# Optimization experiments

Hardware: AMD Instinct MI355X
Metric: run time of the kernel (lower is better)

Reference implementation:

```python
import jax, jax.numpy as jnp
import numpy as np

EPS_SINK = 0.01   # SinkhornDistance eps
N_ITERS = 20      # fixed iteration count (original: max 100 with host-side early exit)
BN_EPS = 1e-5


def _conv(x, w, b):
    # NCHW 3x3 (or 1x1) conv, SAME padding
    y = jax.lax.conv_general_dilated(x, w, (1, 1), 'SAME',
                                     dimension_numbers=('NCHW', 'OIHW', 'NCHW'))
    return y + b[None, :, None, None]


def _bn_train(x, gamma, beta):
    # BatchNorm2d in training mode: batch statistics over (N,H,W)
    m = jnp.mean(x, axis=(0, 2, 3), keepdims=True)
    v = jnp.var(x, axis=(0, 2, 3), keepdims=True)
    return gamma[None, :, None, None] * (x - m) * jax.lax.rsqrt(v + BN_EPS) + beta[None, :, None, None]


def _calc_mean_std(f, eps=1e-5):
    m = jnp.mean(f, axis=(2, 3), keepdims=True)
    s = jnp.sqrt(jnp.var(f, axis=(2, 3), keepdims=True) + eps)
    return m, s


def _sinkhorn_pi(x, y, eps):
    # x: [b, n, d] content points, y: [b, m, d] style points. Cosine-distance cost.
    xn = x / jnp.linalg.norm(x, axis=-1, keepdims=True)
    yn = y / jnp.linalg.norm(y, axis=-1, keepdims=True)
    C = 1.0 - jnp.einsum('bnd,bmd->bnm', xn, yn)          # [b, n, m]
    b, n, m = C.shape
    log_mu = jnp.log(jnp.full((b, n), 1.0 / n) + 1e-8)
    log_nu = jnp.log(jnp.full((b, m), 1.0 / m) + 1e-8)

    def Mmat(u, v):
        # (-C + u_i + v_j) / eps
        return (-C + u[..., None] + v[..., None, :]) / eps

    def step(carry, _):
        u, v = carry
        u = eps * (log_mu - jax.scipy.special.logsumexp(Mmat(u, v), axis=-1)) + u
        v = eps * (log_nu - jax.scipy.special.logsumexp(Mmat(u, v), axis=-2)) + v
        return (u, v), None

    (u, v), _ = jax.lax.scan(step, (jnp.zeros((b, n)), jnp.zeros((b, m))), None, length=N_ITERS)
    return jnp.exp(Mmat(u, v))                             # transport plan pi


def setup_inputs() -> dict:
    key = jax.random.key(0)
    ks = jax.random.split(key, 16)
    bs, dim, h, w = 4, 512, 32, 32
    s = 0.05
    return {
        'content_feat': jax.random.normal(ks[0], (bs, dim, h, w), jnp.float32),
        'style_feat':   jax.random.normal(ks[1], (bs, dim, h, w), jnp.float32),
        # alpha_predictor (version 1): conv(1024->256,3x3) ReLU BN, conv(256->256,3x3) ReLU BN, conv(256->512,3x3)
        'w1': jax.random.normal(ks[2], (256, 1024, 3, 3), jnp.float32) * s,
        'b1': jnp.zeros((256,), jnp.float32),
        'g1': jnp.ones((256,), jnp.float32),
        'be1': jnp.zeros((256,), jnp.float32),
        'w2': jax.random.normal(ks[3], (256, 256, 3, 3), jnp.float32) * s,
        'b2': jnp.zeros((256,), jnp.float32),
        'g2': jnp.ones((256,), jnp.float32),
        'be2': jnp.zeros((256,), jnp.float32),
        'w3': jax.random.normal(ks[4], (512, 256, 3, 3), jnp.float32) * s,
        'b3': jnp.zeros((512,), jnp.float32),
        # stand-in decoder head: 3x3 conv 512->3 (decoder is an external injected module)
        'dec_w': jax.random.normal(ks[5], (3, 512, 3, 3), jnp.float32) * s,
        'dec_b': jnp.zeros((3,), jnp.float32),
    }


def reference(content_feat, style_feat, w1, b1, g1, be1, w2, b2, g2, be2, w3, b3, dec_w, dec_b):
    bs, dim, h, w = content_feat.shape
    cf = content_feat.reshape(bs, dim, h * w).transpose(0, 2, 1)   # [b, hw, d]
    sf = style_feat.reshape(bs, dim, h * w).transpose(0, 2, 1)
    pi = _sinkhorn_pi(cf, sf, EPS_SINK) * (h * w)                  # style_assign: pi * h * w
    t = jnp.einsum('bnm,bmd->bnd', pi, sf).transpose(0, 2, 1).reshape(bs, dim, h, w)
    cm, cs = _calc_mean_std(content_feat)
    c_normed = (content_feat - cm) / cs
    a = _bn_train(jax.nn.relu(_conv(jnp.concatenate([t, content_feat], axis=1), w1, b1)), g1, be1)
    a = _bn_train(jax.nn.relu(_conv(a, w2, b2)), g2, be2)
    alpha = _conv(a, w3, b3)
    t = alpha * c_normed + t
    g_t = _conv(t, dec_w, dec_b)
    return g_t
```

## Files before the change

kernel.cpp:

```cpp
#include <hip/hip_runtime.h>

typedef unsigned short u16;
typedef unsigned int u32;
typedef unsigned long long u64;
typedef float f32x4 __attribute__((ext_vector_type(4)));
typedef short bf16x8 __attribute__((ext_vector_type(8)));

#define DEV static __device__ __forceinline__

DEV float bf2f(u16 u){ union{float f; u32 i;} x; x.i = ((u32)u) << 16; return x.f; }
DEV u16 f2bf(float f){ union{float f; u32 i;} x; x.f = f; u32 u = x.i;
  return (u16)((u + 0x7fffu + ((u >> 16) & 1u)) >> 16); }
DEV u16 f2h(float f){ _Float16 h = (_Float16)f; u16 u; __builtin_memcpy(&u, &h, 2); return u; }
DEV float h2f(u16 u){ _Float16 h; __builtin_memcpy(&h, &u, 2); return (float)h; }
DEV uint4 pack8(const u16* s){ uint4 v;
  v.x = (u32)s[0] | ((u32)s[1]<<16); v.y = (u32)s[2] | ((u32)s[3]<<16);
  v.z = (u32)s[4] | ((u32)s[5]<<16); v.w = (u32)s[6] | ((u32)s[7]<<16); return v; }
DEV f32x4 mfma16(bf16x8 a, bf16x8 b, f32x4 c){
  return __builtin_amdgcn_mfma_f32_16x16x32_bf16(a, b, c, 0, 0, 0);
}
DEV bf16x8 ldfrag(const u16* p){ return *(const bf16x8*)p; }

DEV void st_agent(float* p, float v){
  __hip_atomic_store(p, v, __ATOMIC_RELAXED, __HIP_MEMORY_SCOPE_AGENT); }
DEV float ld_agent(const float* p){
  return __hip_atomic_load(p, __ATOMIC_RELAXED, __HIP_MEMORY_SCOPE_AGENT); }
DEV float2 ld_agent2(const float* p){
  u64 u = __hip_atomic_load((const u64*)p, __ATOMIC_RELAXED, __HIP_MEMORY_SCOPE_AGENT);
  union{u64 u; float2 f;} c; c.u = u; return c.f; }
DEV void st_agent_u32(u32* p, u32 v){
  __hip_atomic_store(p, v, __ATOMIC_RELAXED, __HIP_MEMORY_SCOPE_AGENT); }
DEV u32 ld_agent_u32(const u32* p){
  return __hip_atomic_load(p, __ATOMIC_RELAXED, __HIP_MEMORY_SCOPE_AGENT); }

constexpr float SCL = 144.269504088896341f;
constexpr float LOG2MU = -9.99998522680257f;

constexpr size_t MB = 1ull << 20;
constexpr size_t OFF_G    = 0;
constexpr size_t OFF_GT   = 8*MB;
constexpr size_t OFF_U    = 16*MB;
constexpr size_t OFF_V    = OFF_U   + (16<<10);
constexpr size_t OFF_BAR  = OFF_V   + (16<<10);
constexpr size_t OFF_INS  = OFF_BAR + (16<<10);
constexpr size_t OFF_CNM  = OFF_INS + (16<<10);
constexpr size_t OFF_CNIS = OFF_CNM + (8<<10);
constexpr size_t OFF_BNS  = OFF_CNIS+ (8<<10);
constexpr size_t OFF_PNP  = OFF_BNS + (4<<10);
constexpr size_t OFF_CFH  = 17*MB;
constexpr size_t OFF_CFL  = 21*MB;
constexpr size_t OFF_SFH  = 25*MB;
constexpr size_t OFF_SFL  = 29*MB;
constexpr size_t OFF_SNB  = 33*MB;
constexpr size_t OFF_TN   = 37*MB;
constexpr size_t OFF_TCP  = 45*MB;
constexpr size_t OFF_W1P  = 53*MB;
constexpr size_t OFF_W2P  = OFF_W1P + 9*256*1024*2;
constexpr size_t OFF_W3P  = OFF_W2P + 9*256*256*2;
constexpr size_t OFF_WDP  = OFF_W3P + 9*512*256*2;
constexpr size_t OFF_PIP  = 62*MB;
constexpr size_t OFF_Z1  = 17*MB;
constexpr size_t OFF_A1P = 25*MB;
constexpr size_t OFF_Z2  = 27*MB;
constexpr size_t OFF_A2P = 35*MB;
constexpr size_t OFF_T2P = 17*MB;

__global__ void stats_k(const float* __restrict__ cf, const float* __restrict__ sf,
                        float* __restrict__ cnm, float* __restrict__ cnis,
                        float* __restrict__ part, float* __restrict__ zUV,
                        float* __restrict__ zBNS, u32* __restrict__ zbar,
                        const float* __restrict__ w1, const float* __restrict__ w2,
                        const float* __restrict__ w3, const float* __restrict__ wd,
                        u16* __restrict__ w1p, u16* __restrict__ w2p,
                        u16* __restrict__ w3p, u16* __restrict__ wdp){
  int blk = blockIdx.x;
  if (blk < 2048){
    int bd = blk;
    float4 v = ((const float4*)(cf + (size_t)bd*1024))[threadIdx.x];
    float s = v.x+v.y+v.z+v.w;
    float q = v.x*v.x+v.y*v.y+v.z*v.z+v.w*v.w;
    #pragma unroll
    for (int m = 32; m >= 1; m >>= 1){ s += __shfl_xor(s, m, 64); q += __shfl_xor(q, m, 64); }
    __shared__ float ls[4], lq[4];
    int w = threadIdx.x >> 6;
    if ((threadIdx.x & 63) == 0){ ls[w] = s; lq[w] = q; }
    __syncthreads();
    if (threadIdx.x == 0){
      float S = ls[0]+ls[1]+ls[2]+ls[3], Q = lq[0]+lq[1]+lq[2]+lq[3];
      float mean = S * (1.f/1024.f);
      float var  = Q * (1.f/1024.f) - mean*mean;
      cnm[bd] = mean; cnis[bd] = rsqrtf(var + 1e-5f);
    }
    return;
  }
  if (blk < 2304){
    int rel = blk - 2048;
    int x = rel & 15, y = (rel >> 4) & 7, src = rel >> 7;
    const float* in = src ? sf : cf;
    int p = x*256 + threadIdx.x;
    int b = p >> 10, pp = p & 1023;
    const float* base = in + ((size_t)(b*512 + y*64))*1024 + pp;
    float s = 0.f;
    #pragma unroll 8
    for (int d = 0; d < 64; ++d){ float xx = base[(size_t)d*1024]; s += xx*xx; }
    part[((size_t)(src*8 + y))*4096 + p] = s;
    return;
  }
  if (blk < 2336){
    zUV[(blk - 2304)*256 + threadIdx.x] = 0.f;
    return;
  }
  if (blk < 2340){
    zBNS[(blk - 2336)*256 + threadIdx.x] = 0.f;
    return;
  }
  if (blk < 2356){
    zbar[(blk - 2340)*256 + threadIdx.x] = 0u;
    return;
  }
  int pblk = blk - 2356;
  const float* w; u16* wp; int CI, NCK, rel;
  if (pblk < 512){ w = w1; wp = w1p; CI = 1024; NCK = 32; rel = pblk; }
  else if (pblk < 640){ w = w2; wp = w2p; CI = 256; NCK = 8; rel = pblk - 512; }
  else if (pblk < 896){ w = w3; wp = w3p; CI = 256; NCK = 8; rel = pblk - 640; }
  else {
    int o = (pblk - 896)*256 + threadIdx.x;
    int ci = o & 511; int r = o >> 9; int co = r & 15; int tap = r >> 4;
    wdp[o] = f2bf((co < 3) ? wd[(size_t)(co*512 + ci)*9 + tap] : 0.f);
    return;
  }
  int g = rel / NCK, ck = rel % NCK;
  __shared__ float L[16*288];
  const float* base = w + ((size_t)(g*16)*CI + ck*32)*9;
  #pragma unroll
  for (int i = 0; i < 18; ++i){
    int idx = i*256 + threadIdx.x;
    int row = idx / 288, col = idx - row*288;
    L[row*288 + col] = base[(size_t)row*CI*9 + col];
  }
  __syncthreads();
  u16* dst = wp + ((size_t)(g*NCK + ck)*9)*512;
  #pragma unroll
  for (int i = 0; i < 18; ++i){
    int j = i*256 + threadIdx.x;
    int tap = j >> 9, r = j & 511, lane = r >> 3, e = r & 7;
    int co = lane & 15, cil = ((lane >> 4) & 3)*8 + e;
    dst[j] = f2bf(L[co*288 + cil*9 + tap]);
  }
}

__global__ void tsplit_k(const float* __restrict__ cf, const float* __restrict__ sf,
                         const float* __restrict__ pnp,
                         u16* __restrict__ cfh, u16* __restrict__ cfl,
                         u16* __restrict__ sfh, u16* __restrict__ sfl,
                         u16* __restrict__ tcp, u16* __restrict__ snb){
  __shared__ float tile[64][65];
  int z = blockIdx.z, is_style = z >> 2, b = z & 3;
  const float* src = is_style ? sf : cf;
  u16* hi = is_style ? sfh : cfh;
  u16* lo = is_style ? sfl : cfl;
  int p0 = blockIdx.x*64, d0 = blockIdx.y*64;
  int r = threadIdx.x >> 2, c0 = (threadIdx.x & 3) * 16;
  const float* sp = src + ((size_t)(b*512 + d0 + r))*1024 + p0 + c0;
  float v[16];
  #pragma unroll
  for (int e = 0; e < 4; ++e){
    float4 t4 = ((const float4*)sp)[e];
    v[e*4+0]=t4.x; v[e*4+1]=t4.y; v[e*4+2]=t4.z; v[e*4+3]=t4.w;
  }
  #pragma unroll
  for (int j = 0; j < 16; ++j) tile[r][c0+j] = v[j];
  if (is_style){
    u16 t16[16];
    #pragma unroll
    for (int j = 0; j < 16; ++j) t16[j] = f2bf(v[j]);
    uint4* ap = (uint4*)(snb + ((size_t)(b*512 + d0 + r))*1024 + p0 + c0);
    ap[0] = pack8(t16); ap[1] = pack8(t16+8);
  }
  __syncthreads();
  int pr = r, dc0 = c0;
  float inv;
  {
    const float* pp = pnp + (size_t)(is_style ? 8*4096 : 0) + ((b<<10) + p0 + pr);
    float s = 0.f;
    #pragma unroll
    for (int j = 0; j < 8; ++j) s += pp[j*4096];
    inv = rsqrtf(s);
  }
  u16 h16[16], l16[16], t16[16];
  #pragma unroll
  for (int j = 0; j < 16; ++j){
    float x = tile[dc0+j][pr];
    t16[j] = f2bf(x);
    float xn = x * inv;
    u16 h = f2bf(xn);
    h16[j] = h;
    l16[j] = f2bf(xn - bf2f(h));
  }
  size_t orow = (size_t)((b<<10) + p0 + pr);
  uint4* hp = (uint4*)(hi + orow*512 + d0 + dc0);
  uint4* lp = (uint4*)(lo + orow*512 + d0 + dc0);
  hp[0] = pack8(h16); hp[1] = pack8(h16+8);
  lp[0] = pack8(l16); lp[1] = pack8(l16+8);
  if (!is_style){
    int D = d0 + dc0;
    size_t off = ((size_t)(16 + (D>>5))*4096 + orow)*32 + (D&31);
    *(uint4*)(tcp + off)     = pack8(t16);
    *(uint4*)(tcp + off + 8) = pack8(t16+8);
  }
}

__global__ __launch_bounds__(256) void cgemm_k(const u16* __restrict__ cfh, const u16* __restrict__ cfl,
        const u16* __restrict__ sfh, const u16* __restrict__ sfl,
        u16* __restrict__ G, u16* __restrict__ Gt){
  __shared__ __align__(16) u16 SH[4*128*40];
  u16* Ah = SH;          u16* Al = SH + 5120;
  u16* Bh = SH + 10240;  u16* Bl = SH + 15360;
  int b = blockIdx.z;
  size_t abase = ((size_t)((b<<10) + blockIdx.x*128))*512;
  size_t bbase = ((size_t)((b<<10) + blockIdx.y*128))*512;
  int lane = threadIdx.x & 63, wid = threadIdx.x >> 6;
  int wm = (wid >> 1)*64, wn = (wid & 1)*64;
  int fr = lane & 15, qd = lane >> 4;
  int sr = threadIdx.x >> 1, sc = (threadIdx.x & 1)*16;
  f32x4 acc[4][4] = {};
  for (int kk = 0; kk < 512; kk += 32){
    size_t g0 = (size_t)sr*512 + kk + sc;
    *(uint4*)&Ah[sr*40+sc]   = *(const uint4*)(cfh + abase + g0);
    *(uint4*)&Ah[sr*40+sc+8] = *(const uint4*)(cfh + abase + g0 + 8);
    *(uint4*)&Al[sr*40+sc]   = *(const uint4*)(cfl + abase + g0);
    *(uint4*)&Al[sr*40+sc+8] = *(const uint4*)(cfl + abase + g0 + 8);
    *(uint4*)&Bh[sr*40+sc]   = *(const uint4*)(sfh + bbase + g0);
    *(uint4*)&Bh[sr*40+sc+8] = *(const uint4*)(sfh + bbase + g0 + 8);
    *(uint4*)&Bl[sr*40+sc]   = *(const uint4*)(sfl + bbase + g0);
    *(uint4*)&Bl[sr*40+sc+8] = *(const uint4*)(sfl + bbase + g0 + 8);
    __syncthreads();
    bf16x8 bhf[4], blf[4];
    #pragma unroll
    for (int ni = 0; ni < 4; ++ni){
      bhf[ni] = ldfrag(&Bh[(wn + ni*16 + fr)*40 + qd*8]);
      blf[ni] = ldfrag(&Bl[(wn + ni*16 + fr)*40 + qd*8]);
    }
    #pragma unroll
    for (int mi = 0; mi < 4; ++mi){
      bf16x8 ah = ldfrag(&Ah[(wm + mi*16 + fr)*40 + qd*8]);
      bf16x8 al = ldfrag(&Al[(wm + mi*16 + fr)*40 + qd*8]);
      #pragma unroll
      for (int ni = 0; ni < 4; ++ni){
        acc[mi][ni] = mfma16(ah, bhf[ni], acc[mi][ni]);
        acc[mi][ni] = mfma16(ah, blf[ni], acc[mi][ni]);
        acc[mi][ni] = mfma16(al, bhf[ni], acc[mi][ni]);
      }
    }
    __syncthreads();
  }
  #pragma unroll
  for (int mi = 0; mi < 4; ++mi)
    #pragma unroll
    for (int ni = 0; ni < 4; ++ni)
      #pragma unroll
      for (int rg = 0; rg < 4; ++rg){
        int r = wm + mi*16 + qd*4 + rg;
        int c = wn + ni*16 + fr;
        SH[r*136 + c] = f2h((acc[mi][ni][rg] - 1.f) * SCL);
      }
  __syncthreads();
  size_t gb = (((size_t)b) << 20) + (size_t)(blockIdx.x*128)*1024 + blockIdx.y*128;
  #pragma unroll
  for (int i = 0; i < 8; ++i){
    int idx = i*256 + threadIdx.x;
    int r = idx >> 4, c4 = idx & 15;
    *(uint4*)(G + gb + (size_t)r*1024 + c4*8) = *(const uint4*)&SH[r*136 + c4*8];
  }
  __syncthreads();
  #pragma unroll
  for (int mi = 0; mi < 4; ++mi)
    #pragma unroll
    for (int ni = 0; ni < 4; ++ni)
      #pragma unroll
      for (int rg = 0; rg < 4; ++rg){
        int r = wm + mi*16 + qd*4 + rg;
        int c = wn + ni*16 + fr;
        SH[c*136 + r] = f2h((acc[mi][ni][rg] - 1.f) * SCL);
      }
  __syncthreads();
  size_t gtb = (((size_t)b) << 20) + (size_t)(blockIdx.y*128)*1024 + blockIdx.x*128;
  #pragma unroll
  for (int i = 0; i < 8; ++i){
    int idx = i*256 + threadIdx.x;
    int r = idx >> 4, c4 = idx & 15;
    *(uint4*)(Gt + gtb + (size_t)r*1024 + c4*8) = *(const uint4*)&SH[r*136 + c4*8];
  }
}

__global__ __launch_bounds__(512) void sink_k(const u16* __restrict__ G, const u16* __restrict__ Gt,
        float* __restrict__ U, float* __restrict__ V,
        u32* __restrict__ flags, u16* __restrict__ pip){
  __shared__ __align__(16) u16 LL[2][16*1024];
  int blk = blockIdx.x;
  int b = blk >> 6;
  int sub = blk & 63;
  int rb = sub << 4;
  int tid = threadIdx.x;
  size_t gbase = ((size_t)((b << 10) + rb)) << 10;
  {
    const uint4* g0 = (const uint4*)(G + gbase);
    const uint4* g1 = (const uint4*)(Gt + gbase);
    uint4* d0 = (uint4*)LL[0];
    uint4* d1 = (uint4*)LL[1];
    #pragma unroll
    for (int i = 0; i < 4; ++i){
      d0[i*512 + tid] = g0[i*512 + tid];
      d1[i*512 + tid] = g1[i*512 + tid];
    }
  }
  __syncthreads();
  int wid = tid >> 6, lane = tid & 63;
  float* Ub = U + (b << 10);
  float* Vb = V + (b << 10);
  u32* fgrp = flags + (b << 6)*16;
  u32* fmine = fgrp + sub*16;
  int r0 = wid << 1;
  int cbase = lane << 2;
  int budget = 1 << 21;

  float o0 = 0.f, o1 = 0.f;
  auto dopass = [&](int which, const float* __restrict__ inv, float* __restrict__ outv, int tgt){
    float va[16];
    #pragma unroll
    for (int k = 0; k < 4; ++k){
      #pragma unroll
      for (int j = 0; j < 2; ++j){
        float2 t = ld_agent2(inv + k*256 + cbase + j*2);
        va[k*4 + j*2]     = t.x;
        va[k*4 + j*2 + 1] = t.y;
      }
    }
    #pragma unroll
    for (int rr = 0; rr < 2; ++rr){
      int row = r0 + rr;
      float x[16]; float mx = -3.0e38f;
      #pragma unroll
      for (int k = 0; k < 4; ++k){
        uint2 g2 = *(const uint2*)(&LL[which][row*1024 + k*256 + cbase]);
        float t0 = h2f((u16)(g2.x & 0xffffu)) + va[k*4+0];
        float t1 = h2f((u16)(g2.x >> 16))     + va[k*4+1];
        float t2 = h2f((u16)(g2.y & 0xffffu)) + va[k*4+2];
        float t3 = h2f((u16)(g2.y >> 16))     + va[k*4+3];
        x[k*4+0]=t0; x[k*4+1]=t1; x[k*4+2]=t2; x[k*4+3]=t3;
        mx = fmaxf(mx, fmaxf(fmaxf(t0,t1), fmaxf(t2,t3)));
      }
      #pragma unroll
      for (int m = 32; m >= 1; m >>= 1) mx = fmaxf(mx, __shfl_xor(mx, m, 64));
      float s = 0.f;
      #pragma unroll
      for (int i = 0; i < 16; ++i) s += exp2f(x[i] - mx);
      #pragma unroll
      for (int m = 32; m >= 1; m >>= 1) s += __shfl_xor(s, m, 64);
      float o = LOG2MU - (mx + log2f(s));
      if (rr == 0) o0 = o; else o1 = o;
      if (lane == 0) st_agent(outv + rb + row, o);
    }
    __syncthreads();
    if (tid == 0) st_agent_u32(fmine, (u32)tgt);
    if (tid < 64){
      u32* fl = fgrp + tid*16;
      for (;;){
        u32 v = ld_agent_u32(fl);
        if (__all((int)(v >= (u32)tgt))) break;
        if (--budget < 0) break;
        __builtin_amdgcn_s_sleep(1);
      }
    }
    __syncthreads();
  };

  float ku0 = 0.f, ku1 = 0.f;
  for (int it = 0; it < 20; ++it){
    dopass(0, Vb, Ub, 2*it + 1);
    ku0 = o0; ku1 = o1;
    dopass(1, Ub, Vb, 2*it + 2);
  }

  float va[16];
  #pragma unroll
  for (int k = 0; k < 4; ++k){
    #pragma unroll
    for (int j = 0; j < 2; ++j){
      float2 t = ld_agent2(Vb + k*256 + cbase + j*2);
      va[k*4 + j*2]     = t.x;
      va[k*4 + j*2 + 1] = t.y;
    }
  }
  #pragma unroll
  for (int rr = 0; rr < 2; ++rr){
    int row = r0 + rr;
    float ur = (rr == 0 ? ku0 : ku1) + 10.f;
    size_t orow = ((size_t)((b << 10) + rb + row)) << 10;
    #pragma unroll
    for (int k = 0; k < 4; ++k){
      uint2 g2 = *(const uint2*)(&LL[0][row*1024 + k*256 + cbase]);
      u16 o[4];
      o[0] = f2bf(exp2f(h2f((u16)(g2.x & 0xffffu)) + va[k*4+0] + ur));
      o[1] = f2bf(exp2f(h2f((u16)(g2.x >> 16))     + va[k*4+1] + ur));
      o[2] = f2bf(exp2f(h2f((u16)(g2.y & 0xffffu)) + va[k*4+2] + ur));
      o[3] = f2bf(exp2f(h2f((u16)(g2.y >> 16))     + va[k*4+3] + ur));
      uint2 pk; pk.x = (u32)o[0] | ((u32)o[1]<<16); pk.y = (u32)o[2] | ((u32)o[3]<<16);
      *(uint2*)(pip + orow + k*256 + cbase) = pk;
    }
  }
}

__global__ __launch_bounds__(256) void tgemm_k(const u16* __restrict__ pip,
        const u16* __restrict__ snb, float* __restrict__ tn, u16* __restrict__ tcp){
  __shared__ __align__(16) u16 As[64*40], Bs[128*40];
  int b = blockIdx.z, p0 = blockIdx.x*64, d0 = blockIdx.y*128;
  int tid = threadIdx.x, lane = tid & 63, wid = tid >> 6;
  int wm = (wid >> 1)*32, wn = (wid & 1)*64;
  int fr = lane & 15, qd = lane >> 4;
  int a_r = tid >> 2, a_c = (tid & 3)*8;
  int b_r = tid >> 1, b_c = (tid & 1)*16;
  const u16* Arow = pip + (((size_t)((b<<10) + p0 + a_r)) << 10) + a_c;
  const u16* Brow = snb + (((size_t)(b*512 + d0 + b_r)) << 10) + b_c;
  uint4 pa, pb0, pb1;
  auto issue = [&](int kk){
    pa = *(const uint4*)(Arow + kk);
    const uint4* bp = (const uint4*)(Brow + kk);
    pb0 = bp[0]; pb1 = bp[1];
  };
  f32x4 acc[2][4] = {};
  issue(0);
  for (int kk = 0; kk < 1024; kk += 32){
    *(uint4*)&As[a_r*40 + a_c] = pa;
    *(uint4*)&Bs[b_r*40 + b_c] = pb0;
    *(uint4*)&Bs[b_r*40 + b_c + 8] = pb1;
    __syncthreads();
    if (kk + 32 < 1024) issue(kk + 32);
    bf16x8 bfr[4];
    #pragma unroll
    for (int ni = 0; ni < 4; ++ni) bfr[ni] = ldfrag(&Bs[(wn + ni*16 + fr)*40 + qd*8]);
    #pragma unroll
    for (int mi = 0; mi < 2; ++mi){
      bf16x8 afr = ldfrag(&As[(wm + mi*16 + fr)*40 + qd*8]);
      #pragma unroll
      for (int ni = 0; ni < 4; ++ni) acc[mi][ni] = mfma16(afr, bfr[ni], acc[mi][ni]);
    }
    __syncthreads();
  }
  #pragma unroll
  for (int mi = 0; mi < 2; ++mi)
    #pragma unroll
    for (int ni = 0; ni < 4; ++ni)
      #pragma unroll
      for (int rg = 0; rg < 4; ++rg){
        int p = p0 + wm + mi*16 + qd*4 + rg;
        int d = d0 + wn + ni*16 + fr;
        float vout = acc[mi][ni][rg];
        size_t ro = (size_t)((b<<10) + p);
        tn[ro*512 + d] = vout;
        tcp[((size_t)(d>>5)*4096 + ro)*32 + (d&31)] = f2bf(vout);
      }
}

template<int CI, int CO, int KSPLIT, int MODE>
__global__ __launch_bounds__(256) void conv_k(const u16* __restrict__ inp, const u16* __restrict__ wpk,
        const float* __restrict__ bias, float* __restrict__ fout, u16* __restrict__ bout,
        const u16* __restrict__ tcp, const float* __restrict__ cnm, const float* __restrict__ cnis,
        const float* __restrict__ tn){
  constexpr int NCK_TOT = CI/32, NCK = NCK_TOT/KSPLIT;
  __shared__ __align__(16) u16 As[128*40];
  int b = blockIdx.z & 3, ks = blockIdx.z >> 2;
  int c0 = blockIdx.y*64;
  int r0 = blockIdx.x*2;
  int tid = threadIdx.x, lane = tid & 63, wid = tid >> 6;
  int wm = (wid >> 1)*32, wn = (wid & 1)*32;
  int fr = lane & 15, qd = lane >> 4;
  int ck0 = ks*NCK;
  int hrow = tid >> 1;
  int ah = (tid & 1)*16;
  int gy = r0 - 1 + (hrow >> 5);
  bool a_ok = ((unsigned)gy < 32u);
  size_t arow = (size_t)(b<<10) + (r0-1)*32 + hrow;
  uint4 pa0 = {0,0,0,0}, pa1 = {0,0,0,0};
  auto issueA = [&](int ck){
    if (a_ok){
      const uint4* s = (const uint4*)(inp + ((size_t)(ck0+ck)*4096 + arow)*32 + ah);
      pa0 = s[0]; pa1 = s[1];
    }
  };
  int g0 = (c0 + wn) >> 4;
  const u16* wb0 = wpk + ((size_t)(g0    )*NCK_TOT + ck0)*9*512 + lane*8;
  const u16* wb1 = wpk + ((size_t)(g0 + 1)*NCK_TOT + ck0)*9*512 + lane*8;

  f32x4 acc[2][2] = {};
  issueA(0);
  for (int ck = 0; ck < NCK; ++ck){
    *(uint4*)&As[hrow*40 + ah]     = pa0;
    *(uint4*)&As[hrow*40 + ah + 8] = pa1;
    __syncthreads();
    if (ck + 1 < NCK) issueA(ck + 1);
    #pragma unroll
    for (int tap = 0; tap < 9; ++tap){
      const int dy = tap/3 - 1, dx = tap%3 - 1;
      bf16x8 bf0 = ldfrag(wb0 + (size_t)(ck*9 + tap)*512);
      bf16x8 bf1 = ldfrag(wb1 + (size_t)(ck*9 + tap)*512);
      #pragma unroll
      for (int mi = 0; mi < 2; ++mi){
        int p0w = wm + mi*16;
        int pcol = (p0w & 31) + fr + dx;
        int lr = (p0w >> 5) + dy + 1;
        bool okc = (unsigned)pcol < 32u;
        bf16x8 af = ldfrag(&As[(lr*32 + (okc ? pcol : 0))*40 + qd*8]);
        if (!okc) af = bf16x8(0);
        acc[mi][0] = mfma16(af, bf0, acc[mi][0]);
        acc[mi][1] = mfma16(af, bf1, acc[mi][1]);
      }
    }
    __syncthreads();
  }
  #pragma unroll
  for (int mi = 0; mi < 2; ++mi)
    #pragma unroll
    for (int ni = 0; ni < 2; ++ni)
      #pragma unroll
      for (int rg = 0; rg < 4; ++rg){
        int pp = blockIdx.x*64 + wm + mi*16 + qd*4 + rg;
        int cc = c0 + wn + ni*16 + fr;
        float v = acc[mi][ni][rg];
        size_t ro = (size_t)((b<<10) + pp);
        if (MODE == 0){
          fout[(size_t)ks*4096*CO + ro*CO + cc] = v;
        } else {
          float alpha = v + bias[cc];
          float cn = (bf2f(tcp[((size_t)(16 + (cc>>5))*4096 + ro)*32 + (cc&31)])
                      - cnm[(b<<9) + cc]) * cnis[(b<<9) + cc];
          bout[((size_t)(cc>>5)*4096 + ro)*32 + (cc&31)] = f2bf(alpha*cn + tn[ro*512 + cc]);
        }
      }
}

__global__ __launch_bounds__(512) void dec_k(const u16* __restrict__ t2p, const u16* __restrict__ wdp,
                                             const float* __restrict__ db, float* __restrict__ out){
  __shared__ float wlds[3*4608];
  int tid = threadIdx.x;
  for (int k = tid; k < 3*4608; k += 512){
    int c = k / 4608, rem = k - c*4608;
    int tap = rem >> 9, ci = rem & 511;
    wlds[k] = bf2f(wdp[(size_t)(tap*16 + c)*512 + ci]);
  }
  __syncthreads();
  int b = blockIdx.x >> 5;
  int p = ((blockIdx.x & 31) << 5) + (tid >> 4);
  int sub = tid & 15;
  int py = p >> 5, px = p & 31;
  float a0 = 0.f, a1 = 0.f, a2 = 0.f;
  for (int tap = 0; tap < 9; ++tap){
    int sy = py + tap/3 - 1, sx = px + tap%3 - 1;
    if (((unsigned)sy < 32u) && ((unsigned)sx < 32u)){
      size_t row = (size_t)((b<<10) + (sy<<5) + sx);
      const float* w0 = wlds + tap*512;
      #pragma unroll
      for (int j = 0; j < 4; ++j){
        int ci0 = j*128 + sub*8;
        uint4 v = *(const uint4*)(t2p + ((size_t)(ci0>>5)*4096 + row)*32 + (ci0&31));
        u32 ww[4] = {v.x, v.y, v.z, v.w};
        #pragma unroll
        for (int e = 0; e < 8; ++e){
          float x = bf2f((u16)((e & 1) ? (ww[e>>1] >> 16) : (ww[e>>1] & 0xffffu)));
          a0 += x * w0[ci0 + e];
          a1 += x * w0[4608 + ci0 + e];
          a2 += x * w0[9216 + ci0 + e];
        }
      }
    }
  }
  #pragma unroll
  for (int m = 8; m >= 1; m >>= 1){
    a0 += __shfl_xor(a0, m, 64);
    a1 += __shfl_xor(a1, m, 64);
    a2 += __shfl_xor(a2, m, 64);
  }
  if (sub == 0){
    out[((size_t)(b*3 + 0) << 10) + p] = a0 + db[0];
    out[((size_t)(b*3 + 1) << 10) + p] = a1 + db[1];
    out[((size_t)(b*3 + 2) << 10) + p] = a2 + db[2];
  }
}

__global__ void bn_stats_k(const float* __restrict__ z, const float* __restrict__ bias,
                           float* __restrict__ sums){
  int c = blockIdx.x*64 + (threadIdx.x & 63);
  int w = threadIdx.x >> 6;
  int rbase = blockIdx.y*128 + w*32;
  float bi = bias[c];
  float s = 0.f, q = 0.f;
  for (int i = 0; i < 32; ++i){
    size_t ro = (size_t)(rbase + i)*256 + c;
    float x = fmaxf(z[ro] + z[4096*256 + ro] + bi, 0.f);
    s += x; q += x*x;
  }
  __shared__ float ls[4][64], lq[4][64];
  ls[w][threadIdx.x & 63] = s; lq[w][threadIdx.x & 63] = q;
  __syncthreads();
  if (threadIdx.x < 64){
    float S = ls[0][threadIdx.x]+ls[1][threadIdx.x]+ls[2][threadIdx.x]+ls[3][threadIdx.x];
    float Q = lq[0][threadIdx.x]+lq[1][threadIdx.x]+lq[2][threadIdx.x]+lq[3][threadIdx.x];
    atomicAdd(&sums[blockIdx.x*64 + threadIdx.x], S);
    atomicAdd(&sums[256 + blockIdx.x*64 + threadIdx.x], Q);
  }
}

__global__ void bn_apply_k(const float* __restrict__ z, const float* __restrict__ bias,
                           const float* __restrict__ sums, const float* __restrict__ gamma,
                           const float* __restrict__ beta, u16* __restrict__ ap){
  int idx = blockIdx.x*256 + threadIdx.x;
  float4 va = ((const float4*)z)[idx];
  float4 vb = ((const float4*)(z + 4096*256))[idx];
  int row = idx >> 6;
  int cc0 = (idx << 2) & 255;
  float e[4] = {va.x+vb.x, va.y+vb.y, va.z+vb.z, va.w+vb.w};
  u16 o[4];
  #pragma unroll
  for (int k = 0; k < 4; ++k){
    int c = cc0 + k;
    float mean = sums[c] * (1.f/4096.f);
    float var  = sums[256 + c] * (1.f/4096.f) - mean*mean;
    float sc = gamma[c] * rsqrtf(var + 1e-5f);
    float sh = beta[c] - mean*sc;
    float x = fmaxf(e[k] + bias[c], 0.f);
    o[k] = f2bf(x*sc + sh);
  }
  uint2 pk; pk.x = (u32)o[0] | ((u32)o[1]<<16); pk.y = (u32)o[2] | ((u32)o[3]<<16);
  *(uint2*)(ap + ((size_t)(cc0>>5)*4096 + row)*32 + (cc0&31)) = pk;
}

extern "C" void kernel_launch(void* const* d_in, const int* in_sizes, int n_in,
                              void* d_out, int out_size, void* d_ws, size_t ws_size,
                              hipStream_t stream){
  const float* cf  = (const float*)d_in[0];
  const float* sf  = (const float*)d_in[1];
  const float* w1  = (const float*)d_in[2];
  const float* b1  = (const float*)d_in[3];
  const float* g1  = (const float*)d_in[4];
  const float* be1 = (const float*)d_in[5];
  const float* w2  = (const float*)d_in[6];
  const float* b2  = (const float*)d_in[7];
  const float* g2  = (const float*)d_in[8];
  const float* be2 = (const float*)d_in[9];
  const float* w3  = (const float*)d_in[10];
  const float* b3  = (const float*)d_in[11];
  const float* dw  = (const float*)d_in[12];
  const float* db  = (const float*)d_in[13];

  char* ws = (char*)d_ws;
  u16* G    = (u16*)(ws + OFF_G);
  u16* Gt   = (u16*)(ws + OFF_GT);
  float* U    = (float*)(ws + OFF_U);
  float* V    = (float*)(ws + OFF_V);
  u32* bar    = (u32*)(ws + OFF_BAR);
  float* cnm  = (float*)(ws + OFF_CNM);
  float* cnis = (float*)(ws + OFF_CNIS);
  float* bns1 = (float*)(ws + OFF_BNS);
  float* bns2 = bns1 + 512;
  float* pnp  = (float*)(ws + OFF_PNP);
  u16* cfh = (u16*)(ws + OFF_CFH);
  u16* cfl = (u16*)(ws + OFF_CFL);
  u16* sfh = (u16*)(ws + OFF_SFH);
  u16* sfl = (u16*)(ws + OFF_SFL);
  u16* snb = (u16*)(ws + OFF_SNB);
  float* tn  = (float*)(ws + OFF_TN);
  u16* tcp = (u16*)(ws + OFF_TCP);
  u16* w1p = (u16*)(ws + OFF_W1P);
  u16* w2p = (u16*)(ws + OFF_W2P);
  u16* w3p = (u16*)(ws + OFF_W3P);
  u16* wdp = (u16*)(ws + OFF_WDP);
  u16* pip = (u16*)(ws + OFF_PIP);
  float* z1  = (float*)(ws + OFF_Z1);
  u16*   a1p = (u16*)(ws + OFF_A1P);
  float* z2  = (float*)(ws + OFF_Z2);
  u16*   a2p = (u16*)(ws + OFF_A2P);
  u16*   t2p = (u16*)(ws + OFF_T2P);

  stats_k<<<3540, 256, 0, stream>>>(cf, sf, cnm, cnis, pnp, U, bns1, bar,
                                    w1, w2, w3, dw, w1p, w2p, w3p, wdp);
  tsplit_k<<<dim3(16, 8, 8), 256, 0, stream>>>(cf, sf, pnp, cfh, cfl, sfh, sfl, tcp, snb);

  cgemm_k<<<dim3(8, 8, 4), 256, 0, stream>>>(cfh, cfl, sfh, sfl, G, Gt);

  sink_k<<<256, 512, 0, stream>>>(G, Gt, U, V, bar, pip);

  tgemm_k<<<dim3(16, 4, 4), 256, 0, stream>>>(pip, snb, tn, tcp);

  conv_k<1024, 256, 2, 0><<<dim3(16, 4, 8), 256, 0, stream>>>(
      tcp, w1p, nullptr, z1, nullptr, nullptr, nullptr, nullptr, nullptr);
  bn_stats_k<<<dim3(4, 32), 256, 0, stream>>>(z1, b1, bns1);
  bn_apply_k<<<1024, 256, 0, stream>>>(z1, b1, bns1, g1, be1, a1p);

  conv_k<256, 256, 2, 0><<<dim3(16, 4, 8), 256, 0, stream>>>(
      a1p, w2p, nullptr, z2, nullptr, nullptr, nullptr, nullptr, nullptr);
  bn_stats_k<<<dim3(4, 32), 256, 0, stream>>>(z2, b2, bns2);
  bn_apply_k<<<1024, 256, 0, stream>>>(z2, b2, bns2, g2, be2, a2p);

  conv_k<256, 512, 1, 1><<<dim3(16, 8, 4), 256, 0, stream>>>(
      a2p, w3p, b3, nullptr, t2p, tcp, cnm, cnis, tn);

  dec_k<<<128, 512, 0, stream>>>(t2p, wdp, db, (float*)d_out);

  (void)in_sizes; (void)n_in; (void)out_size; (void)ws_size;
}
```

Before: 393.6 us.

## Overlap content half of conv1 with Sinkhorn blocks; prefetch cgemm tiles

Extra blocks are added to the Sinkhorn kernel launch. They compute the content-channel half of the first 3x3 conv, which depends only on content features, and write it into a second z1 split-K slice while the Sinkhorn blocks iterate. The standalone conv1 launch shrinks its split-K grid to cover only the remaining slice. Separately, the cgemm main loop now register-prefetches the next K tile before computing the current one. The risk is that the Sinkhorn blocks, which use a grid-wide barrier, could be delayed or deadlock if the extra blocks prevent all 256 Sinkhorn blocks from being co-resident.

Result: no change. 389.9 us (-0.9%).

```diff
diff --git a/kernel.cpp b/kernel.cpp
--- a/kernel.cpp
+++ b/kernel.cpp
@@ -23,8 +23,6 @@
 
 DEV void st_agent(float* p, float v){
   __hip_atomic_store(p, v, __ATOMIC_RELAXED, __HIP_MEMORY_SCOPE_AGENT); }
-DEV float ld_agent(const float* p){
-  return __hip_atomic_load(p, __ATOMIC_RELAXED, __HIP_MEMORY_SCOPE_AGENT); }
 DEV float2 ld_agent2(const float* p){
   u64 u = __hip_atomic_load((const u64*)p, __ATOMIC_RELAXED, __HIP_MEMORY_SCOPE_AGENT);
   union{u64 u; float2 f;} c; c.u = u; return c.f; }
@@ -223,18 +221,24 @@
   int wm = (wid >> 1)*64, wn = (wid & 1)*64;
   int fr = lane & 15, qd = lane >> 4;
   int sr = threadIdx.x >> 1, sc = (threadIdx.x & 1)*16;
+  const u16 *pA = cfh + abase, *pB = cfl + abase, *pC = sfh + bbase, *pD = sfl + bbase;
+  uint4 rA0, rA1, rB0, rB1, rC0, rC1, rD0, rD1;
+  auto issue = [&](int kk){
+    size_t g0 = (size_t)sr*512 + kk + sc;
+    rA0 = *(const uint4*)(pA + g0); rA1 = *(const uint4*)(pA + g0 + 8);
+    rB0 = *(const uint4*)(pB + g0); rB1 = *(const uint4*)(pB + g0 + 8);
+    rC0 = *(const uint4*)(pC + g0); rC1 = *(const uint4*)(pC + g0 + 8);
+    rD0 = *(const uint4*)(pD + g0); rD1 = *(const uint4*)(pD + g0 + 8);
+  };
   f32x4 acc[4][4] = {};
+  issue(0);
   for (int kk = 0; kk < 512; kk += 32){
-    size_t g0 = (size_t)sr*512 + kk + sc;
-    *(uint4*)&Ah[sr*40+sc]   = *(const uint4*)(cfh + abase + g0);
-    *(uint4*)&Ah[sr*40+sc+8] = *(const uint4*)(cfh + abase + g0 + 8);
-    *(uint4*)&Al[sr*40+sc]   = *(const uint4*)(cfl + abase + g0);
-    *(uint4*)&Al[sr*40+sc+8] = *(const uint4*)(cfl + abase + g0 + 8);
-    *(uint4*)&Bh[sr*40+sc]   = *(const uint4*)(sfh + bbase + g0);
-    *(uint4*)&Bh[sr*40+sc+8] = *(const uint4*)(sfh + bbase + g0 + 8);
-    *(uint4*)&Bl[sr*40+sc]   = *(const uint4*)(sfl + bbase + g0);
-    *(uint4*)&Bl[sr*40+sc+8] = *(const uint4*)(sfl + bbase + g0 + 8);
-    __syncthreads();
+    *(uint4*)&Ah[sr*40+sc]   = rA0; *(uint4*)&Ah[sr*40+sc+8] = rA1;
+    *(uint4*)&Al[sr*40+sc]   = rB0; *(uint4*)&Al[sr*40+sc+8] = rB1;
+    *(uint4*)&Bh[sr*40+sc]   = rC0; *(uint4*)&Bh[sr*40+sc+8] = rC1;
+    *(uint4*)&Bl[sr*40+sc]   = rD0; *(uint4*)&Bl[sr*40+sc+8] = rD1;
+    __syncthreads();
+    if (kk + 32 < 512) issue(kk + 32);
     bf16x8 bhf[4], blf[4];
     #pragma unroll
     for (int ni = 0; ni < 4; ++ni){
@@ -295,13 +299,68 @@
 
 __global__ __launch_bounds__(512) void sink_k(const u16* __restrict__ G, const u16* __restrict__ Gt,
         float* __restrict__ U, float* __restrict__ V,
-        u32* __restrict__ flags, u16* __restrict__ pip){
+        u32* __restrict__ flags, u16* __restrict__ pip,
+        const u16* __restrict__ cin, const u16* __restrict__ wpk,
+        float* __restrict__ z1out){
   __shared__ __align__(16) u16 LL[2][16*1024];
   int blk = blockIdx.x;
+  int tid = threadIdx.x;
+  if (blk >= 256){
+    u16* As = LL[0];
+    int cbid = blk - 256;
+    int cx = cbid & 15, cy = (cbid >> 4) & 3, b = cbid >> 6;
+    const int NCK_TOT = 32, NCK = 16, ck0 = 16;
+    int c0 = cy*64, r0 = cx*2;
+    int lane = tid & 63, wid = tid >> 6;
+    int wm = (wid >> 2)*32, wn = (wid & 3)*16;
+    int fr = lane & 15, qd = lane >> 4;
+    int hrow = tid >> 2, ah = (tid & 3)*8;
+    int gy = r0 - 1 + (hrow >> 5);
+    bool a_ok = ((unsigned)gy < 32u);
+    size_t arow = (size_t)(b<<10) + (r0-1)*32 + hrow;
+    uint4 pa = {0,0,0,0};
+    auto issueA = [&](int ck){
+      if (a_ok) pa = *(const uint4*)(cin + ((size_t)(ck0+ck)*4096 + arow)*32 + ah);
+    };
+    int g0 = (c0 + wn) >> 4;
+    const u16* wb = wpk + ((size_t)g0*NCK_TOT + ck0)*9*512 + lane*8;
+    f32x4 acc[2] = {};
+    issueA(0);
+    for (int ck = 0; ck < NCK; ++ck){
+      *(uint4*)&As[hrow*40 + ah] = pa;
+      __syncthreads();
+      if (ck + 1 < NCK) issueA(ck + 1);
+      #pragma unroll
+      for (int tap = 0; tap < 9; ++tap){
+        const int dy = tap/3 - 1, dx = tap%3 - 1;
+        bf16x8 bf = ldfrag(wb + (size_t)(ck*9 + tap)*512);
+        #pragma unroll
+        for (int mi = 0; mi < 2; ++mi){
+          int p0w = wm + mi*16;
+          int pcol = (p0w & 31) + fr + dx;
+          int lr = (p0w >> 5) + dy + 1;
+          bool okc = (unsigned)pcol < 32u;
+          bf16x8 af = ldfrag(&As[(lr*32 + (okc ? pcol : 0))*40 + qd*8]);
+          if (!okc) af = bf16x8(0);
+          acc[mi] = mfma16(af, bf, acc[mi]);
+        }
+      }
+      __syncthreads();
+    }
+    #pragma unroll
+    for (int mi = 0; mi < 2; ++mi)
+      #pragma unroll
+      for (int rg = 0; rg < 4; ++rg){
+        int pp = cx*64 + wm + mi*16 + qd*4 + rg;
+        int cc = c0 + wn + fr;
+        size_t ro = (size_t)((b<<10) + pp);
+        z1out[(size_t)4096*256 + ro*256 + cc] = acc[mi][rg];
+      }
+    return;
+  }
   int b = blk >> 6;
   int sub = blk & 63;
   int rb = sub << 4;
-  int tid = threadIdx.x;
   size_t gbase = ((size_t)((b << 10) + rb)) << 10;
   {
     const uint4* g0 = (const uint4*)(G + gbase);
@@ -687,11 +746,11 @@
 
   cgemm_k<<<dim3(8, 8, 4), 256, 0, stream>>>(cfh, cfl, sfh, sfl, G, Gt);
 
-  sink_k<<<256, 512, 0, stream>>>(G, Gt, U, V, bar, pip);
+  sink_k<<<512, 512, 0, stream>>>(G, Gt, U, V, bar, pip, tcp, w1p, z1);
 
   tgemm_k<<<dim3(16, 4, 4), 256, 0, stream>>>(pip, snb, tn, tcp);
 
-  conv_k<1024, 256, 2, 0><<<dim3(16, 4, 8), 256, 0, stream>>>(
+  conv_k<1024, 256, 2, 0><<<dim3(16, 4, 4), 256, 0, stream>>>(
       tcp, w1p, nullptr, z1, nullptr, nullptr, nullptr, nullptr, nullptr);
   bn_stats_k<<<dim3(4, 32), 256, 0, stream>>>(z1, b1, bns1);
   bn_apply_k<<<1024, 256, 0, stream>>>(z1, b1, bns1, g1, be1, a1p);
```
